# Optimization experiments

Measured on AMD Instinct MI355X. Metric: run time of the kernel, lower is better.

Reference implementation:

```python
import jax, jax.numpy as jnp
import numpy as np

S = 8          # nodes per subgraph (last node is the anchor)
B = 8192       # number of subgraphs in the batch
N = B * S      # total nodes
E_PER = S * S  # edges per subgraph (dense local connectivity)
DIN, DOUT = 512, 256
EPS = 1e-12


def _block_edges(key):
    # local src/dst in [0,S) per subgraph, offset to global node ids
    k1, k2 = jax.random.split(key)
    src = jax.random.randint(k1, (B, E_PER), 0, S)
    dst = jax.random.randint(k2, (B, E_PER), 0, S)
    off = (jnp.arange(B) * S)[:, None]
    return (src + off).reshape(-1), (dst + off).reshape(-1)


def setup_inputs() -> dict:
    key = jax.random.key(0)
    ks = jax.random.split(key, 10)
    pos_src, pos_dst = _block_edges(ks[0])
    neg_src, neg_dst = _block_edges(ks[1])
    return {
        "pos_x": jax.random.normal(ks[2], (N, DIN), jnp.float32),
        "neg_x": jax.random.normal(ks[3], (N, DIN), jnp.float32),
        "pos_src": pos_src, "pos_dst": pos_dst,
        "pos_w": jax.random.uniform(ks[4], (B * E_PER,), jnp.float32),
        "neg_src": neg_src, "neg_dst": neg_dst,
        "neg_w": jax.random.uniform(ks[5], (B * E_PER,), jnp.float32),
        "W_gcn": jax.random.normal(ks[6], (DIN, DOUT), jnp.float32) / np.sqrt(DIN),
        "b_gcn": jnp.zeros((DOUT,), jnp.float32),
        "prelu_a": jnp.float32(0.25),
        "W_bil": jax.random.normal(ks[7], (DOUT, DOUT), jnp.float32) / np.sqrt(DOUT),
        "b_bil": jnp.zeros((1,), jnp.float32),
    }


def _l2norm(x):
    return x / jnp.maximum(jnp.linalg.norm(x, axis=1, keepdims=True), EPS)


def _gcn_branch(x, src, dst, w, W_gcn, b_gcn, prelu_a):
    # GraphConv(norm='none') with edge weights: h = A_w (X W) + b
    xw = x @ W_gcn                                      # [N, DOUT]
    agg = jnp.zeros_like(xw).at[dst].add(w[:, None] * xw[src])
    h = agg + b_gcn
    h = jnp.where(h >= 0, h, prelu_a * h)               # PReLU (single param)
    h = h.reshape(B, S, -1)                             # fixed-size subgraphs
    pool = jnp.mean(h[:, :-1], axis=1)                  # mean over non-anchor nodes
    anchor = h[:, -1]                                   # last node per subgraph
    return _l2norm(pool), _l2norm(anchor)


def reference(pos_x, neg_x, pos_src, pos_dst, pos_w, neg_src, neg_dst, neg_w,
              W_gcn, b_gcn, prelu_a, W_bil, b_bil):
    pos_pool, anchor = _gcn_branch(pos_x, pos_src, pos_dst, pos_w, W_gcn, b_gcn, prelu_a)
    neg_pool, _ = _gcn_branch(neg_x, neg_src, neg_dst, neg_w, W_gcn, b_gcn, prelu_a)
    # Bilinear(D, D, 1): score_b = pool_b^T W anchor_b + bias
    pos_scores = jnp.einsum('bd,de,be->b', pos_pool, W_bil, anchor) + b_bil[0]
    neg_scores = jnp.einsum('bd,de,be->b', neg_pool, W_bil, anchor) + b_bil[0]
    return pos_scores, neg_scores
```

## Files before the change

kernel.cpp:

```cpp
#include <hip/hip_runtime.h>
#include <stdint.h>
#include <math.h>

#define SS 8
#define NBLK 8192
#define DIN 512
#define DOUT 256
#define GB 8
#define MT 64
#define BK 32
#define KSTEPS 16
#define VSTR 264
#define EPSN 1e-12f

typedef __bf16 bf16;
typedef __bf16 bf16x8 __attribute__((ext_vector_type(8)));
typedef float  f32x4  __attribute__((ext_vector_type(4)));

typedef __attribute__((address_space(3))) uint32_t       lds_u32;
typedef __attribute__((address_space(1))) const uint32_t g_u32;

__device__ __forceinline__ void dma16(const void* g, void* l) {
    __builtin_amdgcn_global_load_lds((g_u32*)g, (lds_u32*)l, 16, 0, 0);
}

__device__ __forceinline__ bf16x8 cvt8(f32x4 lo, f32x4 hi) {
    bf16x8 r;
    r[0] = (bf16)lo[0]; r[1] = (bf16)lo[1]; r[2] = (bf16)lo[2]; r[3] = (bf16)lo[3];
    r[4] = (bf16)hi[0]; r[5] = (bf16)hi[1]; r[6] = (bf16)hi[2]; r[7] = (bf16)hi[3];
    return r;
}

__global__ void prep_kernel(const float* __restrict__ W_gcn,
                            const float* __restrict__ W_bil,
                            bf16* __restrict__ Wt,
                            bf16* __restrict__ Wh,
                            bf16* __restrict__ Wl) {
    int idx = blockIdx.x * 256 + threadIdx.x;
    if (idx < DIN * DOUT) {
        int k = idx >> 8, n = idx & 255;
        Wt[n * DIN + k] = (bf16)W_gcn[idx];
    } else {
        int j = idx - DIN * DOUT;
        float wv = W_bil[j];
        bf16 h = (bf16)wv;
        Wh[j] = h;
        Wl[j] = (bf16)(wv - (float)h);
    }
}

__global__ __launch_bounds__(256, 2) void cola_fused4(
    const float* __restrict__ pos_x, const float* __restrict__ neg_x,
    const int* __restrict__ pos_src, const int* __restrict__ pos_dst,
    const float* __restrict__ pos_w,
    const int* __restrict__ neg_src, const int* __restrict__ neg_dst,
    const float* __restrict__ neg_w,
    const bf16* __restrict__ Wt, const bf16* __restrict__ Wh,
    const bf16* __restrict__ Wl,
    const float* __restrict__ b_gcn, const float* __restrict__ prelu_a,
    const float* __restrict__ b_bil, float* __restrict__ out)
{
    __shared__ __align__(16) float bufA[2][2][MT * BK];
    __shared__ __align__(16) bf16  bufB[2][DOUT * BK];
    __shared__ float adjP[GB][SS][SS];
    __shared__ float adjN[GB][SS][SS];
    __shared__ float red[5 * GB];

    float* pool_pos = (float*)&bufB[0][0];
    float* v_lds    = pool_pos + GB * DOUT;
    bf16*  ahs      = (bf16*)(v_lds + GB * DOUT);
    bf16*  als      = ahs + GB * VSTR;

    const int t    = threadIdx.x;
    const int wg   = blockIdx.x;
    const int w    = t >> 6;
    const int lane = t & 63;
    const int q    = lane >> 4;
    const int r15  = lane & 15;
    const int row0 = wg * MT;

    for (int i = t; i < GB * 64; i += 256) { ((float*)adjP)[i] = 0.f; ((float*)adjN)[i] = 0.f; }
    if (t < 5 * GB) red[t] = 0.f;
    __syncthreads();

    {
        int2   sp2 = ((const int2*)pos_src)[wg * 256 + t];
        int2   dp2 = ((const int2*)pos_dst)[wg * 256 + t];
        float2 wp2 = ((const float2*)pos_w)[wg * 256 + t];
        int2   sn2 = ((const int2*)neg_src)[wg * 256 + t];
        int2   dn2 = ((const int2*)neg_dst)[wg * 256 + t];
        float2 wn2 = ((const float2*)neg_w)[wg * 256 + t];
        int gl = t >> 5;
        int base = (wg * GB + gl) * SS;
        atomicAdd(&adjP[gl][dp2.x - base][sp2.x - base], wp2.x);
        atomicAdd(&adjP[gl][dp2.y - base][sp2.y - base], wp2.y);
        atomicAdd(&adjN[gl][dn2.x - base][sn2.x - base], wn2.x);
        atomicAdd(&adjN[gl][dn2.y - base][sn2.y - base], wn2.y);
    }

    const int arow_off = lane >> 3;
    const int akq      = (lane & 7) ^ arow_off;
    const int bn_off = lane >> 2;
    const int bkq    = lane & 3;

    auto issue = [&](int s, int bufi) {
        const int kbase = s * BK;
#pragma unroll
        for (int h = 0; h < 2; ++h) {
            int c = w * 2 + h;
            int row = c * 8 + arow_off;
            dma16(pos_x + (size_t)(row0 + row) * DIN + kbase + akq * 4,
                  &bufA[bufi][0][c * 256]);
            dma16(neg_x + (size_t)(row0 + row) * DIN + kbase + akq * 4,
                  &bufA[bufi][1][c * 256]);
        }
#pragma unroll
        for (int j = 0; j < 4; ++j) {
            int c = w * 4 + j;
            dma16(Wt + (size_t)(c * 16 + bn_off) * DIN + kbase + bkq * 8,
                  &bufB[bufi][c * 512]);
        }
    };

    f32x4 accp[4][4], accn[4][4];
#pragma unroll
    for (int mi = 0; mi < 4; ++mi)
#pragma unroll
        for (int ni = 0; ni < 4; ++ni) {
            accp[mi][ni] = (f32x4){0.f, 0.f, 0.f, 0.f};
            accn[mi][ni] = (f32x4){0.f, 0.f, 0.f, 0.f};
        }

    issue(0, 0);
    int cur = 0;
    for (int s = 0; s < KSTEPS; ++s) {
        __syncthreads();
        if (s + 1 < KSTEPS) issue(s + 1, cur ^ 1);

        bf16x8 afp[4], afn[4], bfv[4];
        const int q0 = (2 * q) ^ (r15 & 7);
        const int q1 = q0 ^ 1;
#pragma unroll
        for (int mi = 0; mi < 4; ++mi) {
            int m = mi * 16 + r15;
            f32x4 lo = *(const f32x4*)&bufA[cur][0][m * BK + q0 * 4];
            f32x4 hi = *(const f32x4*)&bufA[cur][0][m * BK + q1 * 4];
            afp[mi] = cvt8(lo, hi);
            lo = *(const f32x4*)&bufA[cur][1][m * BK + q0 * 4];
            hi = *(const f32x4*)&bufA[cur][1][m * BK + q1 * 4];
            afn[mi] = cvt8(lo, hi);
        }
#pragma unroll
        for (int ni = 0; ni < 4; ++ni) {
            int n = w * 64 + ni * 16 + r15;
            bfv[ni] = *(const bf16x8*)&bufB[cur][n * BK + q * 8];
        }
#pragma unroll
        for (int mi = 0; mi < 4; ++mi)
#pragma unroll
            for (int ni = 0; ni < 4; ++ni) {
                accp[mi][ni] = __builtin_amdgcn_mfma_f32_16x16x32_bf16(
                    afp[mi], bfv[ni], accp[mi][ni], 0, 0, 0);
                accn[mi][ni] = __builtin_amdgcn_mfma_f32_16x16x32_bf16(
                    afn[mi], bfv[ni], accn[mi][ni], 0, 0, 0);
            }
        cur ^= 1;
    }
    __syncthreads();

    const float pa = *prelu_a;

#pragma unroll
    for (int mi = 0; mi < 4; ++mi) {
        const int gl = mi * 2 + (q >> 1);
        float part = 0.f;
#pragma unroll
        for (int ni = 0; ni < 4; ++ni) {
            float r0, r1, r2, r3, r4, r5, r6, r7;
#pragma unroll
            for (int r = 0; r < 4; ++r) {
                float own = accp[mi][ni][r];
                float oth = __shfl_xor(own, 16);
                float lo = ((q & 1) == 0) ? own : oth;
                float hi = ((q & 1) == 0) ? oth : own;
                if (r == 0) { r0 = lo; r4 = hi; }
                else if (r == 1) { r1 = lo; r5 = hi; }
                else if (r == 2) { r2 = lo; r6 = hi; }
                else            { r3 = lo; r7 = hi; }
            }
            int c = w * 64 + ni * 16 + r15;
            float bg = b_gcn[c];
            float pool = 0.f, anch = 0.f;
#pragma unroll
            for (int d = 0; d < 8; ++d) {
                const float* ar = &adjP[gl][d][0];
                float a = bg + ar[0]*r0 + ar[1]*r1 + ar[2]*r2 + ar[3]*r3
                             + ar[4]*r4 + ar[5]*r5 + ar[6]*r6 + ar[7]*r7;
                float h = (a >= 0.f) ? a : pa * a;
                if (d < 7) pool += h; else anch = h;
            }
            float pl = pool * (1.f / 7.f);
            if ((q & 1) == 0) {
                pool_pos[gl * DOUT + c] = pl;
                part += pl * pl;
            } else {
                bf16 hh = (bf16)anch;
                ahs[gl * VSTR + c] = hh;
                als[gl * VSTR + c] = (bf16)(anch - (float)hh);
                part += anch * anch;
            }
        }
        part += __shfl_xor(part, 8);
        part += __shfl_xor(part, 4);
        part += __shfl_xor(part, 2);
        part += __shfl_xor(part, 1);
        if (r15 == 0) atomicAdd((q & 1) ? &red[GB + gl] : &red[gl], part);
    }
    __syncthreads();

    {
        f32x4 accv[4];
#pragma unroll
        for (int ni = 0; ni < 4; ++ni) accv[ni] = (f32x4){0.f, 0.f, 0.f, 0.f};
        const int ga = (r15 & 7) * VSTR;
#pragma unroll
        for (int ks = 0; ks < 8; ++ks) {
            bf16x8 ah_f = *(const bf16x8*)(ahs + ga + ks * 32 + q * 8);
            bf16x8 al_f = *(const bf16x8*)(als + ga + ks * 32 + q * 8);
#pragma unroll
            for (int ni = 0; ni < 4; ++ni) {
                int d = w * 64 + ni * 16 + r15;
                bf16x8 bh = *(const bf16x8*)(Wh + (size_t)d * DOUT + ks * 32 + q * 8);
                bf16x8 bl = *(const bf16x8*)(Wl + (size_t)d * DOUT + ks * 32 + q * 8);
                accv[ni] = __builtin_amdgcn_mfma_f32_16x16x32_bf16(ah_f, bh, accv[ni], 0, 0, 0);
                accv[ni] = __builtin_amdgcn_mfma_f32_16x16x32_bf16(al_f, bh, accv[ni], 0, 0, 0);
                accv[ni] = __builtin_amdgcn_mfma_f32_16x16x32_bf16(ah_f, bl, accv[ni], 0, 0, 0);
            }
        }
        float sp[4] = {0.f, 0.f, 0.f, 0.f};
        if (q < 2) {
#pragma unroll
            for (int ni = 0; ni < 4; ++ni) {
                int c = w * 64 + ni * 16 + r15;
#pragma unroll
                for (int r = 0; r < 4; ++r) {
                    int g = q * 4 + r;
                    v_lds[g * DOUT + c] = accv[ni][r];
                    sp[r] += accv[ni][r] * pool_pos[g * DOUT + c];
                }
            }
        }
#pragma unroll
        for (int r = 0; r < 4; ++r) {
            sp[r] += __shfl_xor(sp[r], 8);
            sp[r] += __shfl_xor(sp[r], 4);
            sp[r] += __shfl_xor(sp[r], 2);
            sp[r] += __shfl_xor(sp[r], 1);
        }
        if (q < 2 && r15 == 0) {
#pragma unroll
            for (int r = 0; r < 4; ++r) atomicAdd(&red[3 * GB + q * 4 + r], sp[r]);
        }
    }
    __syncthreads();

#pragma unroll
    for (int mi = 0; mi < 4; ++mi) {
        const int gl = mi * 2 + (q >> 1);
        float part = 0.f;
#pragma unroll
        for (int ni = 0; ni < 4; ++ni) {
            float r0, r1, r2, r3, r4, r5, r6, r7;
#pragma unroll
            for (int r = 0; r < 4; ++r) {
                float own = accn[mi][ni][r];
                float oth = __shfl_xor(own, 16);
                float lo = ((q & 1) == 0) ? own : oth;
                float hi = ((q & 1) == 0) ? oth : own;
                if (r == 0) { r0 = lo; r4 = hi; }
                else if (r == 1) { r1 = lo; r5 = hi; }
                else if (r == 2) { r2 = lo; r6 = hi; }
                else            { r3 = lo; r7 = hi; }
            }
            int c = w * 64 + ni * 16 + r15;
            float bg = b_gcn[c];
            float pool = 0.f;
#pragma unroll
            for (int d = 0; d < 7; ++d) {
                const float* ar = &adjN[gl][d][0];
                float a = bg + ar[0]*r0 + ar[1]*r1 + ar[2]*r2 + ar[3]*r3
                             + ar[4]*r4 + ar[5]*r5 + ar[6]*r6 + ar[7]*r7;
                float h = (a >= 0.f) ? a : pa * a;
                pool += h;
            }
            float pl = pool * (1.f / 7.f);
            part += ((q & 1) == 0) ? pl * v_lds[gl * DOUT + c] : pl * pl;
        }
        part += __shfl_xor(part, 8);
        part += __shfl_xor(part, 4);
        part += __shfl_xor(part, 2);
        part += __shfl_xor(part, 1);
        if (r15 == 0) atomicAdd((q & 1) ? &red[2 * GB + gl] : &red[4 * GB + gl], part);
    }
    __syncthreads();

    if (t < GB) {
        float np = fmaxf(sqrtf(red[t]), EPSN);
        float na = fmaxf(sqrtf(red[GB + t]), EPSN);
        float nn = fmaxf(sqrtf(red[2 * GB + t]), EPSN);
        float bb = b_bil[0];
        out[wg * GB + t]        = red[3 * GB + t] / (np * na) + bb;
        out[NBLK + wg * GB + t] = red[4 * GB + t] / (nn * na) + bb;
    }
}

extern "C" void kernel_launch(void* const* d_in, const int* in_sizes, int n_in,
                              void* d_out, int out_size, void* d_ws, size_t ws_size,
                              hipStream_t stream) {
    const float* pos_x   = (const float*)d_in[0];
    const float* neg_x   = (const float*)d_in[1];
    const int*   pos_src = (const int*)d_in[2];
    const int*   pos_dst = (const int*)d_in[3];
    const float* pos_w   = (const float*)d_in[4];
    const int*   neg_src = (const int*)d_in[5];
    const int*   neg_dst = (const int*)d_in[6];
    const float* neg_w   = (const float*)d_in[7];
    const float* W_gcn   = (const float*)d_in[8];
    const float* b_gcn   = (const float*)d_in[9];
    const float* prelu_a = (const float*)d_in[10];
    const float* W_bil   = (const float*)d_in[11];
    const float* b_bil   = (const float*)d_in[12];
    float* outp = (float*)d_out;

    bf16* Wt = (bf16*)d_ws;
    bf16* Wh = Wt + DIN * DOUT;
    bf16* Wl = Wh + DOUT * DOUT;

    prep_kernel<<<(DIN * DOUT + DOUT * DOUT) / 256, 256, 0, stream>>>(W_gcn, W_bil, Wt, Wh, Wl);
    cola_fused4<<<NBLK / GB, 256, 0, stream>>>(
        pos_x, neg_x, pos_src, pos_dst, pos_w, neg_src, neg_dst, neg_w,
        Wt, Wh, Wl, b_gcn, prelu_a, b_bil, outp);
}
```

Before: 368.7 us.

## Drop LDS staging; each wave owns 16 rows across full output width

```diff
diff --git a/kernel.cpp b/kernel.cpp
--- a/kernel.cpp
+++ b/kernel.cpp
@@ -8,7 +8,6 @@
 #define DOUT 256
 #define GB 8
 #define MT 64
-#define BK 32
 #define KSTEPS 16
 #define VSTR 264
 #define EPSN 1e-12f
@@ -16,13 +15,6 @@
 typedef __bf16 bf16;
 typedef __bf16 bf16x8 __attribute__((ext_vector_type(8)));
 typedef float  f32x4  __attribute__((ext_vector_type(4)));
-
-typedef __attribute__((address_space(3))) uint32_t       lds_u32;
-typedef __attribute__((address_space(1))) const uint32_t g_u32;
-
-__device__ __forceinline__ void dma16(const void* g, void* l) {
-    __builtin_amdgcn_global_load_lds((g_u32*)g, (lds_u32*)l, 16, 0, 0);
-}
 
 __device__ __forceinline__ bf16x8 cvt8(f32x4 lo, f32x4 hi) {
     bf16x8 r;
@@ -49,7 +41,7 @@
     }
 }
 
-__global__ __launch_bounds__(256, 2) void cola_fused4(
+__global__ __launch_bounds__(256, 2) void cola_fused5(
     const float* __restrict__ pos_x, const float* __restrict__ neg_x,
     const int* __restrict__ pos_src, const int* __restrict__ pos_dst,
     const float* __restrict__ pos_w,
@@ -60,16 +52,13 @@
     const float* __restrict__ b_gcn, const float* __restrict__ prelu_a,
     const float* __restrict__ b_bil, float* __restrict__ out)
 {
-    __shared__ __align__(16) float bufA[2][2][MT * BK];
-    __shared__ __align__(16) bf16  bufB[2][DOUT * BK];
     __shared__ float adjP[GB][SS][SS];
     __shared__ float adjN[GB][SS][SS];
     __shared__ float red[5 * GB];
-
-    float* pool_pos = (float*)&bufB[0][0];
-    float* v_lds    = pool_pos + GB * DOUT;
-    bf16*  ahs      = (bf16*)(v_lds + GB * DOUT);
-    bf16*  als      = ahs + GB * VSTR;
+    __shared__ __align__(16) float pool_pos[GB * DOUT];
+    __shared__ __align__(16) float v_lds[GB * DOUT];
+    __shared__ __align__(16) bf16  ahs[GB * VSTR];
+    __shared__ __align__(16) bf16  als[GB * VSTR];
 
     const int t    = threadIdx.x;
     const int wg   = blockIdx.x;
@@ -90,96 +79,75 @@
         int2   sn2 = ((const int2*)neg_src)[wg * 256 + t];
         int2   dn2 = ((const int2*)neg_dst)[wg * 256 + t];
         float2 wn2 = ((const float2*)neg_w)[wg * 256 + t];
-        int gl = t >> 5;
-        int base = (wg * GB + gl) * SS;
-        atomicAdd(&adjP[gl][dp2.x - base][sp2.x - base], wp2.x);
-        atomicAdd(&adjP[gl][dp2.y - base][sp2.y - base], wp2.y);
-        atomicAdd(&adjN[gl][dn2.x - base][sn2.x - base], wn2.x);
-        atomicAdd(&adjN[gl][dn2.y - base][sn2.y - base], wn2.y);
-    }
-
-    const int arow_off = lane >> 3;
-    const int akq      = (lane & 7) ^ arow_off;
-    const int bn_off = lane >> 2;
-    const int bkq    = lane & 3;
-
-    auto issue = [&](int s, int bufi) {
-        const int kbase = s * BK;
-#pragma unroll
-        for (int h = 0; h < 2; ++h) {
-            int c = w * 2 + h;
-            int row = c * 8 + arow_off;
-            dma16(pos_x + (size_t)(row0 + row) * DIN + kbase + akq * 4,
-                  &bufA[bufi][0][c * 256]);
-            dma16(neg_x + (size_t)(row0 + row) * DIN + kbase + akq * 4,
-                  &bufA[bufi][1][c * 256]);
-        }
-#pragma unroll
-        for (int j = 0; j < 4; ++j) {
-            int c = w * 4 + j;
-            dma16(Wt + (size_t)(c * 16 + bn_off) * DIN + kbase + bkq * 8,
-                  &bufB[bufi][c * 512]);
-        }
-    };
-
-    f32x4 accp[4][4], accn[4][4];
-#pragma unroll
-    for (int mi = 0; mi < 4; ++mi)
-#pragma unroll
-        for (int ni = 0; ni < 4; ++ni) {
-            accp[mi][ni] = (f32x4){0.f, 0.f, 0.f, 0.f};
-            accn[mi][ni] = (f32x4){0.f, 0.f, 0.f, 0.f};
-        }
-
-    issue(0, 0);
-    int cur = 0;
+        int gb = t >> 5;
+        int base = (wg * GB + gb) * SS;
+        atomicAdd(&adjP[gb][dp2.x - base][sp2.x - base], wp2.x);
+        atomicAdd(&adjP[gb][dp2.y - base][sp2.y - base], wp2.y);
+        atomicAdd(&adjN[gb][dn2.x - base][sn2.x - base], wn2.x);
+        atomicAdd(&adjN[gb][dn2.y - base][sn2.y - base], wn2.y);
+    }
+
+    const float* aP = pos_x + (size_t)(row0 + w * 16 + r15) * DIN + q * 8;
+    const float* aN = neg_x + (size_t)(row0 + w * 16 + r15) * DIN + q * 8;
+    const bf16*  bW = Wt + (size_t)r15 * DIN + q * 8;
+
+    f32x4 accp[16], accn[16];
+#pragma unroll
+    for (int j = 0; j < 16; ++j) {
+        accp[j] = (f32x4){0.f, 0.f, 0.f, 0.f};
+        accn[j] = (f32x4){0.f, 0.f, 0.f, 0.f};
+    }
+
+    f32x4 pl0 = *(const f32x4*)(aP);
+    f32x4 ph0 = *(const f32x4*)(aP + 4);
+    f32x4 nl0 = *(const f32x4*)(aN);
+    f32x4 nh0 = *(const f32x4*)(aN + 4);
+
     for (int s = 0; s < KSTEPS; ++s) {
-        __syncthreads();
-        if (s + 1 < KSTEPS) issue(s + 1, cur ^ 1);
-
-        bf16x8 afp[4], afn[4], bfv[4];
-        const int q0 = (2 * q) ^ (r15 & 7);
-        const int q1 = q0 ^ 1;
-#pragma unroll
-        for (int mi = 0; mi < 4; ++mi) {
-            int m = mi * 16 + r15;
-            f32x4 lo = *(const f32x4*)&bufA[cur][0][m * BK + q0 * 4];
-            f32x4 hi = *(const f32x4*)&bufA[cur][0][m * BK + q1 * 4];
-            afp[mi] = cvt8(lo, hi);
-            lo = *(const f32x4*)&bufA[cur][1][m * BK + q0 * 4];
-            hi = *(const f32x4*)&bufA[cur][1][m * BK + q1 * 4];
-            afn[mi] = cvt8(lo, hi);
-        }
-#pragma unroll
-        for (int ni = 0; ni < 4; ++ni) {
-            int n = w * 64 + ni * 16 + r15;
-            bfv[ni] = *(const bf16x8*)&bufB[cur][n * BK + q * 8];
-        }
-#pragma unroll
-        for (int mi = 0; mi < 4; ++mi)
-#pragma unroll
-            for (int ni = 0; ni < 4; ++ni) {
-                accp[mi][ni] = __builtin_amdgcn_mfma_f32_16x16x32_bf16(
-                    afp[mi], bfv[ni], accp[mi][ni], 0, 0, 0);
-                accn[mi][ni] = __builtin_amdgcn_mfma_f32_16x16x32_bf16(
-                    afn[mi], bfv[ni], accn[mi][ni], 0, 0, 0);
-            }
-        cur ^= 1;
+        const int s2 = (s + 1 < KSTEPS) ? s + 1 : s;
+        f32x4 pl1 = *(const f32x4*)(aP + s2 * 32);
+        f32x4 ph1 = *(const f32x4*)(aP + s2 * 32 + 4);
+        f32x4 nl1 = *(const f32x4*)(aN + s2 * 32);
+        f32x4 nh1 = *(const f32x4*)(aN + s2 * 32 + 4);
+
+        bf16x8 b0[8];
+#pragma unroll
+        for (int j = 0; j < 8; ++j)
+            b0[j] = *(const bf16x8*)(bW + (size_t)(j * 16) * DIN + s * 32);
+
+        bf16x8 afp = cvt8(pl0, ph0);
+        bf16x8 afn = cvt8(nl0, nh0);
+
+        bf16x8 b1[8];
+#pragma unroll
+        for (int j = 0; j < 8; ++j)
+            b1[j] = *(const bf16x8*)(bW + (size_t)((j + 8) * 16) * DIN + s * 32);
+
+#pragma unroll
+        for (int j = 0; j < 8; ++j) {
+            accp[j] = __builtin_amdgcn_mfma_f32_16x16x32_bf16(afp, b0[j], accp[j], 0, 0, 0);
+            accn[j] = __builtin_amdgcn_mfma_f32_16x16x32_bf16(afn, b0[j], accn[j], 0, 0, 0);
+        }
+#pragma unroll
+        for (int j = 0; j < 8; ++j) {
+            accp[j + 8] = __builtin_amdgcn_mfma_f32_16x16x32_bf16(afp, b1[j], accp[j + 8], 0, 0, 0);
+            accn[j + 8] = __builtin_amdgcn_mfma_f32_16x16x32_bf16(afn, b1[j], accn[j + 8], 0, 0, 0);
+        }
+        pl0 = pl1; ph0 = ph1; nl0 = nl1; nh0 = nh1;
     }
     __syncthreads();
 
     const float pa = *prelu_a;
-
-#pragma unroll
-    for (int mi = 0; mi < 4; ++mi) {
-        const int gl = mi * 2 + (q >> 1);
+    const int gl = 2 * w + (q >> 1);
+
+    {
         float part = 0.f;
 #pragma unroll
-        for (int ni = 0; ni < 4; ++ni) {
+        for (int ni = 0; ni < 16; ++ni) {
             float r0, r1, r2, r3, r4, r5, r6, r7;
 #pragma unroll
             for (int r = 0; r < 4; ++r) {
-                float own = accp[mi][ni][r];
+                float own = accp[ni][r];
                 float oth = __shfl_xor(own, 16);
                 float lo = ((q & 1) == 0) ? own : oth;
                 float hi = ((q & 1) == 0) ? oth : own;
@@ -188,7 +156,7 @@
                 else if (r == 2) { r2 = lo; r6 = hi; }
                 else            { r3 = lo; r7 = hi; }
             }
-            int c = w * 64 + ni * 16 + r15;
+            int c = ni * 16 + r15;
             float bg = b_gcn[c];
             float pool = 0.f, anch = 0.f;
 #pragma unroll
@@ -214,7 +182,7 @@
         part += __shfl_xor(part, 4);
         part += __shfl_xor(part, 2);
         part += __shfl_xor(part, 1);
-        if (r15 == 0) atomicAdd((q & 1) ? &red[GB + gl] : &red[gl], part);
+        if (r15 == 0) { if (q & 1) red[GB + gl] = part; else red[gl] = part; }
     }
     __syncthreads();
 
@@ -264,16 +232,14 @@
     }
     __syncthreads();
 
-#pragma unroll
-    for (int mi = 0; mi < 4; ++mi) {
-        const int gl = mi * 2 + (q >> 1);
+    {
         float part = 0.f;
 #pragma unroll
-        for (int ni = 0; ni < 4; ++ni) {
+        for (int ni = 0; ni < 16; ++ni) {
             float r0, r1, r2, r3, r4, r5, r6, r7;
 #pragma unroll
             for (int r = 0; r < 4; ++r) {
-                float own = accn[mi][ni][r];
+                float own = accn[ni][r];
                 float oth = __shfl_xor(own, 16);
                 float lo = ((q & 1) == 0) ? own : oth;
                 float hi = ((q & 1) == 0) ? oth : own;
@@ -282,7 +248,7 @@
                 else if (r == 2) { r2 = lo; r6 = hi; }
                 else            { r3 = lo; r7 = hi; }
             }
-            int c = w * 64 + ni * 16 + r15;
+            int c = ni * 16 + r15;
             float bg = b_gcn[c];
             float pool = 0.f;
 #pragma unroll
@@ -300,7 +266,7 @@
         part += __shfl_xor(part, 4);
         part += __shfl_xor(part, 2);
         part += __shfl_xor(part, 1);
-        if (r15 == 0) atomicAdd((q & 1) ? &red[2 * GB + gl] : &red[4 * GB + gl], part);
+        if (r15 == 0) { if (q & 1) red[2 * GB + gl] = part; else red[4 * GB + gl] = part; }
     }
     __syncthreads();
 
@@ -337,7 +303,7 @@
     bf16* Wl = Wh + DOUT * DOUT;
 
     prep_kernel<<<(DIN * DOUT + DOUT * DOUT) / 256, 256, 0, stream>>>(W_gcn, W_bil, Wt, Wh, Wl);
-    cola_fused4<<<NBLK / GB, 256, 0, stream>>>(
+    cola_fused5<<<NBLK / GB, 256, 0, stream>>>(
         pos_x, neg_x, pos_src, pos_dst, pos_w, neg_src, neg_dst, neg_w,
         Wt, Wh, Wl, b_gcn, prelu_a, b_bil, outp);
 }
```

Measured after the change: 451.4 us. 1.22x slower.

## Triple-buffer activation tiles and load pre-tiled weights directly into registers

Applied to the files above, without the earlier changes.

```diff
diff --git a/kernel.cpp b/kernel.cpp
--- a/kernel.cpp
+++ b/kernel.cpp
@@ -39,7 +39,7 @@
     int idx = blockIdx.x * 256 + threadIdx.x;
     if (idx < DIN * DOUT) {
         int k = idx >> 8, n = idx & 255;
-        Wt[n * DIN + k] = (bf16)W_gcn[idx];
+        Wt[((size_t)(k >> 5) * DOUT + n) * BK + (k & 31)] = (bf16)W_gcn[idx];
     } else {
         int j = idx - DIN * DOUT;
         float wv = W_bil[j];
@@ -49,7 +49,7 @@
     }
 }
 
-__global__ __launch_bounds__(256, 2) void cola_fused4(
+__global__ __launch_bounds__(256, 2) void cola_fused6(
     const float* __restrict__ pos_x, const float* __restrict__ neg_x,
     const int* __restrict__ pos_src, const int* __restrict__ pos_dst,
     const float* __restrict__ pos_w,
@@ -60,15 +60,14 @@
     const float* __restrict__ b_gcn, const float* __restrict__ prelu_a,
     const float* __restrict__ b_bil, float* __restrict__ out)
 {
-    __shared__ __align__(16) float bufA[2][2][MT * BK];
-    __shared__ __align__(16) bf16  bufB[2][DOUT * BK];
+    __shared__ __align__(16) float bufA[3][2][MT * BK];
     __shared__ float adjP[GB][SS][SS];
     __shared__ float adjN[GB][SS][SS];
     __shared__ float red[5 * GB];
 
-    float* pool_pos = (float*)&bufB[0][0];
+    float* pool_pos = (float*)&bufA[0][0][0];
     float* v_lds    = pool_pos + GB * DOUT;
-    bf16*  ahs      = (bf16*)(v_lds + GB * DOUT);
+    bf16*  ahs      = (bf16*)&bufA[1][0][0];
     bf16*  als      = ahs + GB * VSTR;
 
     const int t    = threadIdx.x;
@@ -100,10 +99,8 @@
 
     const int arow_off = lane >> 3;
     const int akq      = (lane & 7) ^ arow_off;
-    const int bn_off = lane >> 2;
-    const int bkq    = lane & 3;
-
-    auto issue = [&](int s, int bufi) {
+
+    auto issueA = [&](int s, int bufi) {
         const int kbase = s * BK;
 #pragma unroll
         for (int h = 0; h < 2; ++h) {
@@ -114,12 +111,13 @@
             dma16(neg_x + (size_t)(row0 + row) * DIN + kbase + akq * 4,
                   &bufA[bufi][1][c * 256]);
         }
-#pragma unroll
-        for (int j = 0; j < 4; ++j) {
-            int c = w * 4 + j;
-            dma16(Wt + (size_t)(c * 16 + bn_off) * DIN + kbase + bkq * 8,
-                  &bufB[bufi][c * 512]);
-        }
+    };
+
+    auto loadB = [&](bf16x8* dst, int s) {
+#pragma unroll
+        for (int ni = 0; ni < 4; ++ni)
+            dst[ni] = *(const bf16x8*)(Wt +
+                ((size_t)s * DOUT + w * 64 + ni * 16 + r15) * BK + q * 8);
     };
 
     f32x4 accp[4][4], accn[4][4];
@@ -131,29 +129,38 @@
             accn[mi][ni] = (f32x4){0.f, 0.f, 0.f, 0.f};
         }
 
-    issue(0, 0);
-    int cur = 0;
+    bf16x8 breg[2][4];
+
+    issueA(0, 0);
+    loadB(breg[0], 0);
+    issueA(1, 1);
+
+#pragma unroll
     for (int s = 0; s < KSTEPS; ++s) {
-        __syncthreads();
-        if (s + 1 < KSTEPS) issue(s + 1, cur ^ 1);
-
-        bf16x8 afp[4], afn[4], bfv[4];
+        if (s == KSTEPS - 1)
+            asm volatile("s_waitcnt vmcnt(0) lgkmcnt(0)" ::: "memory");
+        else
+            asm volatile("s_waitcnt vmcnt(4) lgkmcnt(0)" ::: "memory");
+        __builtin_amdgcn_s_barrier();
+        __builtin_amdgcn_sched_barrier(0);
+
+        if (s + 1 < KSTEPS) loadB(breg[(s + 1) & 1], s + 1);
+        if (s + 2 < KSTEPS) issueA(s + 2, (s + 2) % 3);
+
+        const int bufi = s % 3;
+        const bf16x8* bfv = breg[s & 1];
         const int q0 = (2 * q) ^ (r15 & 7);
         const int q1 = q0 ^ 1;
+        bf16x8 afp[4], afn[4];
 #pragma unroll
         for (int mi = 0; mi < 4; ++mi) {
             int m = mi * 16 + r15;
-            f32x4 lo = *(const f32x4*)&bufA[cur][0][m * BK + q0 * 4];
-            f32x4 hi = *(const f32x4*)&bufA[cur][0][m * BK + q1 * 4];
+            f32x4 lo = *(const f32x4*)&bufA[bufi][0][m * BK + q0 * 4];
+            f32x4 hi = *(const f32x4*)&bufA[bufi][0][m * BK + q1 * 4];
             afp[mi] = cvt8(lo, hi);
-            lo = *(const f32x4*)&bufA[cur][1][m * BK + q0 * 4];
-            hi = *(const f32x4*)&bufA[cur][1][m * BK + q1 * 4];
+            lo = *(const f32x4*)&bufA[bufi][1][m * BK + q0 * 4];
+            hi = *(const f32x4*)&bufA[bufi][1][m * BK + q1 * 4];
             afn[mi] = cvt8(lo, hi);
-        }
-#pragma unroll
-        for (int ni = 0; ni < 4; ++ni) {
-            int n = w * 64 + ni * 16 + r15;
-            bfv[ni] = *(const bf16x8*)&bufB[cur][n * BK + q * 8];
         }
 #pragma unroll
         for (int mi = 0; mi < 4; ++mi)
@@ -164,7 +171,6 @@
                 accn[mi][ni] = __builtin_amdgcn_mfma_f32_16x16x32_bf16(
                     afn[mi], bfv[ni], accn[mi][ni], 0, 0, 0);
             }
-        cur ^= 1;
     }
     __syncthreads();
 
@@ -337,7 +343,7 @@
     bf16* Wl = Wh + DOUT * DOUT;
 
     prep_kernel<<<(DIN * DOUT + DOUT * DOUT) / 256, 256, 0, stream>>>(W_gcn, W_bil, Wt, Wh, Wl);
-    cola_fused4<<<NBLK / GB, 256, 0, stream>>>(
+    cola_fused6<<<NBLK / GB, 256, 0, stream>>>(
         pos_x, neg_x, pos_src, pos_dst, pos_w, neg_src, neg_dst, neg_w,
         Wt, Wh, Wl, b_gcn, prelu_a, b_bil, outp);
 }
```

Measured after the change: 366.3 us. No clear change (-0.7%).
